# Optimization experiments

Hardware: AMD Instinct MI355X
Metric: run time of the kernel (lower is better)

The kernel has to match this reference:

```python
import jax, jax.numpy as jnp
import numpy as np
from jax import lax

B, NP = 4, 8192          # events, points per event (equal-sized batches)
RATIO, R, K = 0.25, 0.2, 64
MP = int(NP * RATIO)     # sampled centers per event
D_IN = 32
BIG = 1e10


def _fps_one(pos):
    # Farthest point sampling (deterministic start at index 0). pos: [NP,3] -> [MP] int32
    d = jnp.sum((pos - pos[0]) ** 2, axis=-1)
    sel = jnp.zeros((MP,), jnp.int32)

    def body(i, carry):
        sel, d = carry
        nxt = jnp.argmax(d).astype(jnp.int32)
        sel = sel.at[i].set(nxt)
        d = jnp.minimum(d, jnp.sum((pos - pos[nxt]) ** 2, axis=-1))
        return sel, d

    sel, _ = lax.fori_loop(1, MP, body, (sel, d))
    return sel


def _ball_query_one(centers, pos):
    # centers: [MP,3], pos: [NP,3] -> neighbor idx [MP,K] int32, validity mask [MP,K]
    d2 = jnp.sum((centers[:, None, :] - pos[None, :, :]) ** 2, axis=-1)  # [MP,NP]
    d2m = jnp.where(d2 <= R * R, d2, BIG)
    neg, idx = lax.top_k(-d2m, K)          # K nearest within radius (deterministic)
    mask = (-neg) <= R * R
    return idx.astype(jnp.int32), mask


def reference(x, pos, batch, W1, b1, W2, b2, W3, b3):
    xb = x.reshape(B, NP, D_IN)
    pb = pos.reshape(B, NP, 3)

    sel = jax.vmap(_fps_one)(pb)                                   # [B,MP]
    centers = jnp.take_along_axis(pb, sel[..., None], axis=1)      # [B,MP,3]
    idx, mask = jax.vmap(_ball_query_one)(centers, pb)             # [B,MP,K]

    gather = jax.vmap(lambda a, i: a[i])
    pos_j = gather(pb, idx)                                        # [B,MP,K,3]
    x_j = gather(xb, idx)                                          # [B,MP,K,D_IN]

    rel = pos_j - centers[:, :, None, :]
    h = jnp.concatenate([x_j, rel], axis=-1)                       # [B,MP,K,D_IN+3]
    h = jax.nn.relu(h @ W1 + b1)
    h = jax.nn.relu(h @ W2 + b2)
    h = jax.nn.relu(h @ W3 + b3)                                   # [B,MP,K,128]

    h = jnp.where(mask[..., None], h, -BIG)
    x_out = jnp.max(h, axis=2).reshape(B * MP, -1)                 # max aggregation
    pos_out = centers.reshape(B * MP, 3)
    batch_out = jnp.repeat(jnp.arange(B, dtype=jnp.int32), MP)
    return x_out, pos_out, batch_out


def setup_inputs() -> dict:
    key = jax.random.key(0)
    ks = jax.random.split(key, 8)
    x = jax.random.normal(ks[0], (B * NP, D_IN), jnp.float32)
    pos = jax.random.uniform(ks[1], (B * NP, 3), jnp.float32)
    batch = (jnp.arange(B * NP) // NP).astype(jnp.int64)
    W1 = jax.random.normal(ks[2], (D_IN + 3, 64), jnp.float32) * 0.05
    b1 = jnp.zeros((64,), jnp.float32)
    W2 = jax.random.normal(ks[3], (64, 64), jnp.float32) * 0.05
    b2 = jnp.zeros((64,), jnp.float32)
    W3 = jax.random.normal(ks[4], (64, 128), jnp.float32) * 0.05
    b3 = jnp.zeros((128,), jnp.float32)
    return {"x": x, "pos": pos, "batch": batch, "W1": W1, "b1": b1,
            "W2": W2, "b2": b2, "W3": W3, "b3": b3}
```

## Files before the change

### kernel.cpp

```cpp
#include <hip/hip_runtime.h>


#define BATCH 4
#define NP 8192
#define MP 2048
#define KNN 64
#define DIN 32

#define DPP_FMAX(v, ctrl)                                                     \
  {                                                                           \
    int _t = __builtin_amdgcn_update_dpp(__float_as_int(v),                   \
                                         __float_as_int(v), (ctrl), 0xF,      \
                                         0xF, false);                         \
    (v) = fmaxf((v), __int_as_float(_t));                                     \
  }

#define DPP_MINU(v, ctrl)                                                     \
  {                                                                           \
    unsigned _t = (unsigned)__builtin_amdgcn_update_dpp((int)(v), (int)(v),   \
                                                        (ctrl), 0xF, 0xF,    \
                                                        false);               \
    (v) = ((v) < _t) ? (v) : _t;                                              \
  }

#define DPP_WAVEMAX6(v)                                                       \
  {                                                                           \
    DPP_FMAX(v, 0x111);                                                       \
    DPP_FMAX(v, 0x112);                                                       \
    DPP_FMAX(v, 0x114);                                                       \
    DPP_FMAX(v, 0x118);                                                       \
    DPP_FMAX(v, 0x142);                                                       \
    DPP_FMAX(v, 0x143);                                                       \
  }

typedef float v2f __attribute__((ext_vector_type(2)));

__global__ __launch_bounds__(1024) void fps_k(const float* __restrict__ pos,
                                              const float* __restrict__ x,
                                              const float* __restrict__ W1,
                                              const float* __restrict__ W2,
                                              const float* __restrict__ W3,
                                              float* __restrict__ pout,
                                              float* __restrict__ bout,
                                              float* __restrict__ P1,
                                              float* __restrict__ W2T,
                                              float* __restrict__ W3T)
{
  const int bid = blockIdx.x;
  const int tid = threadIdx.x;

  if (bid >= BATCH) {
    if (bid < BATCH + 2048) {
      const int j = (bid - BATCH) * 16 + (tid >> 6);
      const int c = tid & 63;
      const float* __restrict__ xr = x + (size_t)j * DIN;
      float acc = 0.f;
#pragma unroll
      for (int k = 0; k < DIN; k++) acc += xr[k] * W1[k * 64 + c];
      P1[(size_t)j * 64 + c] = acc;
    } else {
#pragma unroll
      for (int it = 0; it < 12; it++) {
        const int e = it * 1024 + tid;
        if (e < 64 * 64) {
          const int c = e >> 6, k = e & 63;
          W2T[e] = W2[k * 64 + c];
        } else {
          const int e2 = e - 64 * 64;
          const int c = e2 >> 6, k = e2 & 63;
          W3T[e2] = W3[k * 128 + c];
        }
      }
    }
    return;
  }

  const int b = bid;
  const int lane = tid & 63, wid = tid >> 6;
  const float* __restrict__ pb = pos + (size_t)b * NP * 3;
  const int base = tid * 8;

  bout[b * MP + tid] = (float)b;
  bout[b * MP + 1024 + tid] = (float)b;

  __shared__ __align__(16) float ptab[NP * 3];
  __shared__ unsigned long long slt[2][16];

  float t[24];
  const float4* __restrict__ pv = (const float4*)(pb + (size_t)tid * 24);
#pragma unroll
  for (int q = 0; q < 6; q++) *(float4*)&t[q * 4] = pv[q];
#pragma unroll
  for (int q = 0; q < 6; q++) *(float4*)&ptab[tid * 24 + q * 4] = *(float4*)&t[q * 4];

  v2f px[4], py[4], pz[4], d[4];
#pragma unroll
  for (int j = 0; j < 4; j++) {
    px[j].x = t[6 * j + 0]; py[j].x = t[6 * j + 1]; pz[j].x = t[6 * j + 2];
    px[j].y = t[6 * j + 3]; py[j].y = t[6 * j + 4]; pz[j].y = t[6 * j + 5];
  }

  const float c0x = pb[0], c0y = pb[1], c0z = pb[2];
  if (tid == 0) {
    pout[(size_t)b * MP * 3 + 0] = c0x;
    pout[(size_t)b * MP * 3 + 1] = c0y;
    pout[(size_t)b * MP * 3 + 2] = c0z;
  }

  float bv = -1.f;
  {
    v2f cx = {c0x, c0x}, cy = {c0y, c0y}, cz = {c0z, c0z};
#pragma unroll
    for (int j = 0; j < 4; j++) {
      v2f dx = px[j] - cx, dy = py[j] - cy, dz = pz[j] - cz;
      v2f nd = dx * dx + dy * dy + dz * dz;
      d[j] = nd;
      bv = fmaxf(bv, fmaxf(nd.x, nd.y));
    }
  }

  for (int i = 1; i < MP; i++) {
    float v = bv;
    DPP_WAVEMAX6(v);
    const float wmax =
        __int_as_float(__builtin_amdgcn_readlane(__float_as_int(v), 63));

    const unsigned long long m = __ballot(bv == wmax);
    const int src = (int)__builtin_ctzll(m);
    const int p = i & 1;
    if (lane == src) {
      int ks = 7;
#pragma unroll
      for (int k = 6; k >= 0; k--) {
        float dv = (k & 1) ? d[k >> 1].y : d[k >> 1].x;
        if (dv == wmax) ks = k;
      }
      slt[p][wid] = ((unsigned long long)__float_as_uint(wmax) << 32)
                    | (unsigned)(base + ks);
    }
    __syncthreads();

    const unsigned long long kv = slt[p][lane & 15];
    const float v2 = __uint_as_float((unsigned)(kv >> 32));
    float v2r = v2;
    DPP_FMAX(v2r, 0x111);
    DPP_FMAX(v2r, 0x112);
    DPP_FMAX(v2r, 0x114);
    DPP_FMAX(v2r, 0x118);
    const float mv =
        __int_as_float(__builtin_amdgcn_readlane(__float_as_int(v2r), 15));
    const unsigned long long m2 = __ballot(v2 == mv);
    const int mw = (int)__builtin_ctzll(m2);
    const int js = __builtin_amdgcn_readlane((int)(unsigned)kv, mw);
    const float ncx = ptab[js * 3 + 0];
    const float ncy = ptab[js * 3 + 1];
    const float ncz = ptab[js * 3 + 2];

    if (tid == 0) {
      pout[((size_t)b * MP + i) * 3 + 0] = ncx;
      pout[((size_t)b * MP + i) * 3 + 1] = ncy;
      pout[((size_t)b * MP + i) * 3 + 2] = ncz;
    }

    const v2f cx = {ncx, ncx}, cy = {ncy, ncy}, cz = {ncz, ncz};
    bv = -1.f;
#pragma unroll
    for (int j = 0; j < 4; j++) {
      v2f dx = px[j] - cx, dy = py[j] - cy, dz = pz[j] - cz;
      v2f nd = dx * dx + dy * dy + dz * dz;
      v2f dn;
      dn.x = fminf(d[j].x, nd.x);
      dn.y = fminf(d[j].y, nd.y);
      d[j] = dn;
      bv = fmaxf(bv, fmaxf(dn.x, dn.y));
    }
  }
}

__global__ __launch_bounds__(64) void bqmlp_k(const float* __restrict__ pos,
    const float* __restrict__ P1, const float* __restrict__ W1,
    const float* __restrict__ b1, const float* __restrict__ W2T,
    const float* __restrict__ b2, const float* __restrict__ W3T,
    const float* __restrict__ b3, const float* __restrict__ pout,
    float* __restrict__ xout)
{
  __shared__ unsigned long long cand[1024];

  const int wg = blockIdx.x;
  const int lane = threadIdx.x;
  const int b = wg >> 11;
  const float* __restrict__ pb = pos + (size_t)b * NP * 3;
  const float cx = pout[(size_t)wg * 3 + 0];
  const float cy = pout[(size_t)wg * 3 + 1];
  const float cz = pout[(size_t)wg * 3 + 2];
  const float R2 = (float)(0.2 * 0.2);

  int cnt = 0;
  for (int basej = 0; basej < NP; basej += 64) {
    const int j = basej + lane;
    float dx = pb[j * 3 + 0] - cx;
    float dy = pb[j * 3 + 1] - cy;
    float dz = pb[j * 3 + 2] - cz;
    float d2 = dx * dx + dy * dy + dz * dz;
    bool in = (d2 <= R2);
    unsigned long long mb = __ballot(in);
    int pre = (int)__popcll(mb & ((1ull << lane) - 1ull));
    int slot = cnt + pre;
    if (in && slot < 1024)
      cand[slot] = ((unsigned long long)__float_as_uint(d2) << 32) | (unsigned int)j;
    cnt += (int)__popcll(mb);
  }
  if (cnt > 1024) cnt = 1024;

  unsigned long long last = 0;
  int myout = -1;
  for (int r = 0; r < KNN; r++) {
    unsigned long long v = ~0ull;
    for (int s = lane; s < cnt; s += 64) {
      const unsigned long long c = cand[s];
      if (c >= last && c < v) v = c;
    }
    const unsigned hi = (unsigned)(v >> 32);
    unsigned h = hi;
    DPP_MINU(h, 0x111);
    DPP_MINU(h, 0x112);
    DPP_MINU(h, 0x114);
    DPP_MINU(h, 0x118);
    DPP_MINU(h, 0x142);
    DPP_MINU(h, 0x143);
    const unsigned mhi = (unsigned)__builtin_amdgcn_readlane((int)h, 63);
    const unsigned lo = (hi == mhi) ? (unsigned)v : 0xffffffffu;
    unsigned l2 = lo;
    DPP_MINU(l2, 0x111);
    DPP_MINU(l2, 0x112);
    DPP_MINU(l2, 0x114);
    DPP_MINU(l2, 0x118);
    DPP_MINU(l2, 0x142);
    DPP_MINU(l2, 0x143);
    const unsigned mlo = (unsigned)__builtin_amdgcn_readlane((int)l2, 63);

    if (lane == r) myout = (mhi == 0xffffffffu) ? -1 : (int)mlo;
    last = (mhi == 0xffffffffu)
               ? ~0ull
               : ((((unsigned long long)mhi << 32) | mlo) + 1ull);
  }

  const int idx = myout;
  const bool valid = idx >= 0;
  const int j = valid ? idx : 0;
  const float* __restrict__ pj = pos + ((size_t)b * NP + j) * 3;
  const float rx = pj[0] - cx, ry = pj[1] - cy, rz = pj[2] - cz;
  const float* __restrict__ p1r =
      (const float*)__builtin_assume_aligned(P1 + ((size_t)b * NP + j) * 64, 16);

  float h1[64];
#pragma unroll
  for (int k = 0; k < 64; k++) {
    float v = p1r[k] + rx * W1[32 * 64 + k] + ry * W1[33 * 64 + k]
                     + rz * W1[34 * 64 + k] + b1[k];
    h1[k] = fmaxf(v, 0.f);
  }

  float h2[64];
#pragma unroll
  for (int c = 0; c < 64; c++) {
    float a = b2[c];
    const float* __restrict__ w = W2T + c * 64;
#pragma unroll
    for (int k = 0; k < 64; k++) a += h1[k] * w[k];
    h2[c] = fmaxf(a, 0.f);
  }

  float4 keep = make_float4(0.f, 0.f, 0.f, 0.f);
  for (int pass = 0; pass < 4; pass++) {
    const float* __restrict__ wp = W3T + (size_t)(pass * 32) * 64;
    const float* __restrict__ bp = b3 + pass * 32;
    float acc[32];
#pragma unroll
    for (int g = 0; g < 32; g++) acc[g] = bp[g];
#pragma unroll
    for (int k = 0; k < 64; k++) {
      const float hk = h2[k];
#pragma unroll
      for (int g = 0; g < 32; g++) acc[g] += hk * wp[g * 64 + k];
    }
#pragma unroll
    for (int g4 = 0; g4 < 8; g4++) {
      float a0 = valid ? fmaxf(acc[g4 * 4 + 0], 0.f) : 0.f;
      float a1 = valid ? fmaxf(acc[g4 * 4 + 1], 0.f) : 0.f;
      float a2 = valid ? fmaxf(acc[g4 * 4 + 2], 0.f) : 0.f;
      float a3 = valid ? fmaxf(acc[g4 * 4 + 3], 0.f) : 0.f;
      DPP_WAVEMAX6(a0);
      DPP_WAVEMAX6(a1);
      DPP_WAVEMAX6(a2);
      DPP_WAVEMAX6(a3);
      const float m0 =
          __int_as_float(__builtin_amdgcn_readlane(__float_as_int(a0), 63));
      const float m1 =
          __int_as_float(__builtin_amdgcn_readlane(__float_as_int(a1), 63));
      const float m2 =
          __int_as_float(__builtin_amdgcn_readlane(__float_as_int(a2), 63));
      const float m3 =
          __int_as_float(__builtin_amdgcn_readlane(__float_as_int(a3), 63));
      const int cch = pass * 8 + g4;
      if (lane == cch) {
        keep.x = m0; keep.y = m1; keep.z = m2; keep.w = m3;
      }
    }
  }
  if (lane < 32)
    *(float4*)&xout[(size_t)wg * 128 + lane * 4] = keep;
}

extern "C" void kernel_launch(void* const* d_in, const int* in_sizes, int n_in,
                              void* d_out, int out_size, void* d_ws, size_t ws_size,
                              hipStream_t stream)
{
  const float* x   = (const float*)d_in[0];
  const float* pos = (const float*)d_in[1];
  const float* W1 = (const float*)d_in[3];
  const float* b1 = (const float*)d_in[4];
  const float* W2 = (const float*)d_in[5];
  const float* b2 = (const float*)d_in[6];
  const float* W3 = (const float*)d_in[7];
  const float* b3 = (const float*)d_in[8];

  float* out  = (float*)d_out;
  float* xout = out;
  float* pout = out + 8192 * 128;
  float* bout = out + 8192 * 128 + 8192 * 3;

  char* ws = (char*)d_ws;
  float* P1  = (float*)ws;
  float* W2T = (float*)(ws + 8388608);
  float* W3T = (float*)(ws + 8404992);

  fps_k<<<dim3(BATCH + 2048 + 1), dim3(1024), 0, stream>>>(
      pos, x, W1, W2, W3, pout, bout, P1, W2T, W3T);
  bqmlp_k<<<dim3(BATCH * MP), dim3(64), 0, stream>>>(pos, P1, W1, b1, W2T, b2,
                                                     W3T, b3, pout, xout);
}
```

Before: 2.475 ms.

## Fuse FPS and ball-query MLP into persistent kernel overlapping via progress flags

```diff
diff --git a/kernel.cpp b/kernel.cpp
--- a/kernel.cpp
+++ b/kernel.cpp
@@ -6,6 +6,9 @@
 #define MP 2048
 #define KNN 64
 #define DIN 32
+#define NWORK 200
+#define NBLK (BATCH + NWORK)
+#define CAND_CAP 512
 
 #define DPP_FMAX(v, ctrl)                                                     \
   {                                                                           \
@@ -25,291 +28,311 @@
 
 #define DPP_WAVEMAX6(v)                                                       \
   {                                                                           \
-    DPP_FMAX(v, 0x111);                                                       \
-    DPP_FMAX(v, 0x112);                                                       \
-    DPP_FMAX(v, 0x114);                                                       \
-    DPP_FMAX(v, 0x118);                                                       \
-    DPP_FMAX(v, 0x142);                                                       \
-    DPP_FMAX(v, 0x143);                                                       \
+    DPP_FMAX(v, 0x111); DPP_FMAX(v, 0x112); DPP_FMAX(v, 0x114);               \
+    DPP_FMAX(v, 0x118); DPP_FMAX(v, 0x142); DPP_FMAX(v, 0x143);               \
+  }
+
+#define DPP_WAVEMINU6(v)                                                      \
+  {                                                                           \
+    DPP_MINU(v, 0x111); DPP_MINU(v, 0x112); DPP_MINU(v, 0x114);               \
+    DPP_MINU(v, 0x118); DPP_MINU(v, 0x142); DPP_MINU(v, 0x143);               \
   }
 
 typedef float v2f __attribute__((ext_vector_type(2)));
 
-__global__ __launch_bounds__(1024) void fps_k(const float* __restrict__ pos,
-                                              const float* __restrict__ x,
-                                              const float* __restrict__ W1,
-                                              const float* __restrict__ W2,
-                                              const float* __restrict__ W3,
-                                              float* __restrict__ pout,
-                                              float* __restrict__ bout,
-                                              float* __restrict__ P1,
-                                              float* __restrict__ W2T,
-                                              float* __restrict__ W3T)
+__device__ __forceinline__ int aload(const int* p) {
+  return __hip_atomic_load(p, __ATOMIC_RELAXED, __HIP_MEMORY_SCOPE_AGENT);
+}
+
+__global__ void init_k(int* __restrict__ flags) {
+  if (threadIdx.x < 8) flags[threadIdx.x] = 0;
+}
+
+__global__ __launch_bounds__(1024) void mega_k(const float* __restrict__ pos,
+                                               const float* __restrict__ x,
+                                               const float* __restrict__ W1,
+                                               const float* __restrict__ b1,
+                                               const float* __restrict__ W2,
+                                               const float* __restrict__ b2,
+                                               const float* __restrict__ W3,
+                                               const float* __restrict__ b3,
+                                               float* __restrict__ pout,
+                                               float* __restrict__ bout,
+                                               float* __restrict__ P1,
+                                               float* __restrict__ W2T,
+                                               float* __restrict__ xout,
+                                               int* __restrict__ flags)
 {
+  __shared__ __align__(16) float smem[NP * 3];
+  __shared__ unsigned long long slt[2][16];
+
+  int* const prog   = flags;
+  int* const ticket = flags + 4;
+  int* const p1done = flags + 5;
+
   const int bid = blockIdx.x;
   const int tid = threadIdx.x;
-
-  if (bid >= BATCH) {
-    if (bid < BATCH + 2048) {
-      const int j = (bid - BATCH) * 16 + (tid >> 6);
-      const int c = tid & 63;
+  const int lane = tid & 63, wid = tid >> 6;
+
+  if (bid < BATCH) {
+    const int b = bid;
+    float* const ptab = smem;
+    const float* __restrict__ pb = pos + (size_t)b * NP * 3;
+    const int base = tid * 8;
+
+    bout[b * MP + tid] = (float)b;
+    bout[b * MP + 1024 + tid] = (float)b;
+
+    float t[24];
+    const float4* __restrict__ pv = (const float4*)(pb + (size_t)tid * 24);
+#pragma unroll
+    for (int q = 0; q < 6; q++) *(float4*)&t[q * 4] = pv[q];
+#pragma unroll
+    for (int q = 0; q < 6; q++)
+      *(float4*)&ptab[tid * 24 + q * 4] = *(float4*)&t[q * 4];
+
+    v2f px[4], py[4], pz[4], d[4];
+#pragma unroll
+    for (int j = 0; j < 4; j++) {
+      px[j].x = t[6 * j + 0]; py[j].x = t[6 * j + 1]; pz[j].x = t[6 * j + 2];
+      px[j].y = t[6 * j + 3]; py[j].y = t[6 * j + 4]; pz[j].y = t[6 * j + 5];
+    }
+
+    const float c0x = pb[0], c0y = pb[1], c0z = pb[2];
+    if (tid == 0) {
+      pout[(size_t)b * MP * 3 + 0] = c0x;
+      pout[(size_t)b * MP * 3 + 1] = c0y;
+      pout[(size_t)b * MP * 3 + 2] = c0z;
+    }
+
+    float bv = -1.f;
+    {
+      v2f cx = {c0x, c0x}, cy = {c0y, c0y}, cz = {c0z, c0z};
+#pragma unroll
+      for (int j = 0; j < 4; j++) {
+        v2f dx = px[j] - cx, dy = py[j] - cy, dz = pz[j] - cz;
+        v2f nd = dx * dx + dy * dy + dz * dz;
+        d[j] = nd;
+        bv = fmaxf(bv, fmaxf(nd.x, nd.y));
+      }
+    }
+
+    for (int i = 1; i < MP; i++) {
+      float v = bv;
+      DPP_WAVEMAX6(v);
+      const float wmax =
+          __int_as_float(__builtin_amdgcn_readlane(__float_as_int(v), 63));
+
+      const unsigned long long m = __ballot(bv == wmax);
+      const int src = (int)__builtin_ctzll(m);
+      const int p = i & 1;
+      if (lane == src) {
+        int ks = 7;
+#pragma unroll
+        for (int k = 6; k >= 0; k--) {
+          float dv = (k & 1) ? d[k >> 1].y : d[k >> 1].x;
+          if (dv == wmax) ks = k;
+        }
+        slt[p][wid] = ((unsigned long long)__float_as_uint(wmax) << 32)
+                      | (unsigned)(base + ks);
+      }
+      __syncthreads();
+
+      const unsigned long long kv = slt[p][lane & 15];
+      const float v2 = __uint_as_float((unsigned)(kv >> 32));
+      float v2r = v2;
+      DPP_FMAX(v2r, 0x111);
+      DPP_FMAX(v2r, 0x112);
+      DPP_FMAX(v2r, 0x114);
+      DPP_FMAX(v2r, 0x118);
+      const float mv =
+          __int_as_float(__builtin_amdgcn_readlane(__float_as_int(v2r), 15));
+      const unsigned long long m2 = __ballot(v2 == mv);
+      const int mw = (int)__builtin_ctzll(m2);
+      const int js = __builtin_amdgcn_readlane((int)(unsigned)kv, mw);
+      const float ncx = ptab[js * 3 + 0];
+      const float ncy = ptab[js * 3 + 1];
+      const float ncz = ptab[js * 3 + 2];
+
+      if (tid == 0) {
+        pout[((size_t)b * MP + i) * 3 + 0] = ncx;
+        pout[((size_t)b * MP + i) * 3 + 1] = ncy;
+        pout[((size_t)b * MP + i) * 3 + 2] = ncz;
+        if ((i & 31) == 31) {
+          __threadfence();
+          __hip_atomic_store(&prog[b], i + 1, __ATOMIC_RELEASE,
+                             __HIP_MEMORY_SCOPE_AGENT);
+        }
+      }
+
+      const v2f cx = {ncx, ncx}, cy = {ncy, ncy}, cz = {ncz, ncz};
+      bv = -1.f;
+#pragma unroll
+      for (int j = 0; j < 4; j++) {
+        v2f dx = px[j] - cx, dy = py[j] - cy, dz = pz[j] - cz;
+        v2f nd = dx * dx + dy * dy + dz * dz;
+        v2f dn;
+        dn.x = fminf(d[j].x, nd.x);
+        dn.y = fminf(d[j].y, nd.y);
+        d[j] = dn;
+        bv = fmaxf(bv, fmaxf(dn.x, dn.y));
+      }
+    }
+    return;
+  }
+
+  {
+    const int wbid = bid - BATCH;
+    for (size_t e = (size_t)wbid * 1024 + tid; e < (size_t)32768 * 64;
+         e += (size_t)NWORK * 1024) {
+      const int j = (int)(e >> 6), c = (int)(e & 63);
       const float* __restrict__ xr = x + (size_t)j * DIN;
       float acc = 0.f;
 #pragma unroll
       for (int k = 0; k < DIN; k++) acc += xr[k] * W1[k * 64 + c];
       P1[(size_t)j * 64 + c] = acc;
-    } else {
-#pragma unroll
-      for (int it = 0; it < 12; it++) {
-        const int e = it * 1024 + tid;
-        if (e < 64 * 64) {
-          const int c = e >> 6, k = e & 63;
-          W2T[e] = W2[k * 64 + c];
-        } else {
-          const int e2 = e - 64 * 64;
-          const int c = e2 >> 6, k = e2 & 63;
-          W3T[e2] = W3[k * 128 + c];
+    }
+    if (bid == BATCH) {
+      for (int e = tid; e < 64 * 64; e += 1024) {
+        const int c = e >> 6, k = e & 63;
+        W2T[e] = W2[k * 64 + c];
+      }
+    }
+    __syncthreads();
+    if (tid == 0) { __threadfence(); atomicAdd(p1done, 1); }
+  }
+
+  unsigned long long* const cw =
+      (unsigned long long*)smem + (size_t)wid * CAND_CAP;
+  const float R2 = (float)(0.2 * 0.2);
+  bool mlp_ready = false;
+
+  for (;;) {
+    int t;
+    if (lane == 0) t = atomicAdd(ticket, 1);
+    t = __builtin_amdgcn_readfirstlane(t);
+    if (t >= BATCH * MP) break;
+    const int b = t & 3;
+    const int cIdx = t >> 2;
+    const int wg = b * MP + cIdx;
+
+    while (aload(&prog[b]) < cIdx + 1) __builtin_amdgcn_s_sleep(32);
+    __threadfence();
+
+    const float* __restrict__ pb = pos + (size_t)b * NP * 3;
+    const float cx = pout[(size_t)wg * 3 + 0];
+    const float cy = pout[(size_t)wg * 3 + 1];
+    const float cz = pout[(size_t)wg * 3 + 2];
+
+    int cnt = 0;
+    for (int basej = 0; basej < NP; basej += 64) {
+      const int j = basej + lane;
+      float dx = pb[j * 3 + 0] - cx;
+      float dy = pb[j * 3 + 1] - cy;
+      float dz = pb[j * 3 + 2] - cz;
+      float d2 = dx * dx + dy * dy + dz * dz;
+      bool in = (d2 <= R2);
+      unsigned long long mb = __ballot(in);
+      int pre = (int)__popcll(mb & ((1ull << lane) - 1ull));
+      int slot = cnt + pre;
+      if (in && slot < CAND_CAP)
+        cw[slot] = ((unsigned long long)__float_as_uint(d2) << 32)
+                   | (unsigned int)j;
+      cnt += (int)__popcll(mb);
+    }
+    if (cnt > CAND_CAP) cnt = CAND_CAP;
+
+    unsigned long long last = 0;
+    int myout = -1;
+    for (int r = 0; r < KNN; r++) {
+      unsigned long long v = ~0ull;
+      for (int s = lane; s < cnt; s += 64) {
+        const unsigned long long c = cw[s];
+        if (c >= last && c < v) v = c;
+      }
+      const unsigned hi = (unsigned)(v >> 32);
+      unsigned h = hi;
+      DPP_WAVEMINU6(h);
+      const unsigned mhi = (unsigned)__builtin_amdgcn_readlane((int)h, 63);
+      const unsigned lo = (hi == mhi) ? (unsigned)v : 0xffffffffu;
+      unsigned l2 = lo;
+      DPP_WAVEMINU6(l2);
+      const unsigned mlo = (unsigned)__builtin_amdgcn_readlane((int)l2, 63);
+      if (lane == r) myout = (mhi == 0xffffffffu) ? -1 : (int)mlo;
+      last = (mhi == 0xffffffffu)
+                 ? ~0ull
+                 : ((((unsigned long long)mhi << 32) | mlo) + 1ull);
+    }
+
+    if (!mlp_ready) {
+      while (aload(p1done) < NWORK) __builtin_amdgcn_s_sleep(32);
+      __threadfence();
+      mlp_ready = true;
+    }
+
+    const int idx = myout;
+    const bool valid = idx >= 0;
+    const int j = valid ? idx : 0;
+    const float* __restrict__ pj = pos + ((size_t)b * NP + j) * 3;
+    const float rx = pj[0] - cx, ry = pj[1] - cy, rz = pj[2] - cz;
+    const float* __restrict__ p1r = (const float*)__builtin_assume_aligned(
+        P1 + ((size_t)b * NP + j) * 64, 16);
+
+    float h1[64];
+#pragma unroll
+    for (int k = 0; k < 64; k++) {
+      float vv = p1r[k] + rx * W1[32 * 64 + k] + ry * W1[33 * 64 + k]
+                        + rz * W1[34 * 64 + k] + b1[k];
+      h1[k] = fmaxf(vv, 0.f);
+    }
+
+    float4 keep = make_float4(0.f, 0.f, 0.f, 0.f);
+    for (int pass = 0; pass < 4; pass++) {
+      float acc[32];
+#pragma unroll
+      for (int g = 0; g < 32; g++) acc[g] = b3[pass * 32 + g];
+#pragma unroll 2
+      for (int c = 0; c < 64; c++) {
+        const float* __restrict__ w = W2T + c * 64;
+        float a0 = 0.f, a1 = 0.f, a2 = 0.f, a3 = 0.f;
+#pragma unroll
+        for (int k4 = 0; k4 < 16; k4++) {
+          a0 += h1[k4 * 4 + 0] * w[k4 * 4 + 0];
+          a1 += h1[k4 * 4 + 1] * w[k4 * 4 + 1];
+          a2 += h1[k4 * 4 + 2] * w[k4 * 4 + 2];
+          a3 += h1[k4 * 4 + 3] * w[k4 * 4 + 3];
         }
-      }
-    }
-    return;
-  }
-
-  const int b = bid;
-  const int lane = tid & 63, wid = tid >> 6;
-  const float* __restrict__ pb = pos + (size_t)b * NP * 3;
-  const int base = tid * 8;
-
-  bout[b * MP + tid] = (float)b;
-  bout[b * MP + 1024 + tid] = (float)b;
-
-  __shared__ __align__(16) float ptab[NP * 3];
-  __shared__ unsigned long long slt[2][16];
-
-  float t[24];
-  const float4* __restrict__ pv = (const float4*)(pb + (size_t)tid * 24);
-#pragma unroll
-  for (int q = 0; q < 6; q++) *(float4*)&t[q * 4] = pv[q];
-#pragma unroll
-  for (int q = 0; q < 6; q++) *(float4*)&ptab[tid * 24 + q * 4] = *(float4*)&t[q * 4];
-
-  v2f px[4], py[4], pz[4], d[4];
-#pragma unroll
-  for (int j = 0; j < 4; j++) {
-    px[j].x = t[6 * j + 0]; py[j].x = t[6 * j + 1]; pz[j].x = t[6 * j + 2];
-    px[j].y = t[6 * j + 3]; py[j].y = t[6 * j + 4]; pz[j].y = t[6 * j + 5];
-  }
-
-  const float c0x = pb[0], c0y = pb[1], c0z = pb[2];
-  if (tid == 0) {
-    pout[(size_t)b * MP * 3 + 0] = c0x;
-    pout[(size_t)b * MP * 3 + 1] = c0y;
-    pout[(size_t)b * MP * 3 + 2] = c0z;
-  }
-
-  float bv = -1.f;
-  {
-    v2f cx = {c0x, c0x}, cy = {c0y, c0y}, cz = {c0z, c0z};
-#pragma unroll
-    for (int j = 0; j < 4; j++) {
-      v2f dx = px[j] - cx, dy = py[j] - cy, dz = pz[j] - cz;
-      v2f nd = dx * dx + dy * dy + dz * dz;
-      d[j] = nd;
-      bv = fmaxf(bv, fmaxf(nd.x, nd.y));
-    }
-  }
-
-  for (int i = 1; i < MP; i++) {
-    float v = bv;
-    DPP_WAVEMAX6(v);
-    const float wmax =
-        __int_as_float(__builtin_amdgcn_readlane(__float_as_int(v), 63));
-
-    const unsigned long long m = __ballot(bv == wmax);
-    const int src = (int)__builtin_ctzll(m);
-    const int p = i & 1;
-    if (lane == src) {
-      int ks = 7;
-#pragma unroll
-      for (int k = 6; k >= 0; k--) {
-        float dv = (k & 1) ? d[k >> 1].y : d[k >> 1].x;
-        if (dv == wmax) ks = k;
-      }
-      slt[p][wid] = ((unsigned long long)__float_as_uint(wmax) << 32)
-                    | (unsigned)(base + ks);
-    }
-    __syncthreads();
-
-    const unsigned long long kv = slt[p][lane & 15];
-    const float v2 = __uint_as_float((unsigned)(kv >> 32));
-    float v2r = v2;
-    DPP_FMAX(v2r, 0x111);
-    DPP_FMAX(v2r, 0x112);
-    DPP_FMAX(v2r, 0x114);
-    DPP_FMAX(v2r, 0x118);
-    const float mv =
-        __int_as_float(__builtin_amdgcn_readlane(__float_as_int(v2r), 15));
-    const unsigned long long m2 = __ballot(v2 == mv);
-    const int mw = (int)__builtin_ctzll(m2);
-    const int js = __builtin_amdgcn_readlane((int)(unsigned)kv, mw);
-    const float ncx = ptab[js * 3 + 0];
-    const float ncy = ptab[js * 3 + 1];
-    const float ncz = ptab[js * 3 + 2];
-
-    if (tid == 0) {
-      pout[((size_t)b * MP + i) * 3 + 0] = ncx;
-      pout[((size_t)b * MP + i) * 3 + 1] = ncy;
-      pout[((size_t)b * MP + i) * 3 + 2] = ncz;
-    }
-
-    const v2f cx = {ncx, ncx}, cy = {ncy, ncy}, cz = {ncz, ncz};
-    bv = -1.f;
-#pragma unroll
-    for (int j = 0; j < 4; j++) {
-      v2f dx = px[j] - cx, dy = py[j] - cy, dz = pz[j] - cz;
-      v2f nd = dx * dx + dy * dy + dz * dz;
-      v2f dn;
-      dn.x = fminf(d[j].x, nd.x);
-      dn.y = fminf(d[j].y, nd.y);
-      d[j] = dn;
-      bv = fmaxf(bv, fmaxf(dn.x, dn.y));
-    }
-  }
-}
-
-__global__ __launch_bounds__(64) void bqmlp_k(const float* __restrict__ pos,
-    const float* __restrict__ P1, const float* __restrict__ W1,
-    const float* __restrict__ b1, const float* __restrict__ W2T,
-    const float* __restrict__ b2, const float* __restrict__ W3T,
-    const float* __restrict__ b3, const float* __restrict__ pout,
-    float* __restrict__ xout)
-{
-  __shared__ unsigned long long cand[1024];
-
-  const int wg = blockIdx.x;
-  const int lane = threadIdx.x;
-  const int b = wg >> 11;
-  const float* __restrict__ pb = pos + (size_t)b * NP * 3;
-  const float cx = pout[(size_t)wg * 3 + 0];
-  const float cy = pout[(size_t)wg * 3 + 1];
-  const float cz = pout[(size_t)wg * 3 + 2];
-  const float R2 = (float)(0.2 * 0.2);
-
-  int cnt = 0;
-  for (int basej = 0; basej < NP; basej += 64) {
-    const int j = basej + lane;
-    float dx = pb[j * 3 + 0] - cx;
-    float dy = pb[j * 3 + 1] - cy;
-    float dz = pb[j * 3 + 2] - cz;
-    float d2 = dx * dx + dy * dy + dz * dz;
-    bool in = (d2 <= R2);
-    unsigned long long mb = __ballot(in);
-    int pre = (int)__popcll(mb & ((1ull << lane) - 1ull));
-    int slot = cnt + pre;
-    if (in && slot < 1024)
-      cand[slot] = ((unsigned long long)__float_as_uint(d2) << 32) | (unsigned int)j;
-    cnt += (int)__popcll(mb);
-  }
-  if (cnt > 1024) cnt = 1024;
-
-  unsigned long long last = 0;
-  int myout = -1;
-  for (int r = 0; r < KNN; r++) {
-    unsigned long long v = ~0ull;
-    for (int s = lane; s < cnt; s += 64) {
-      const unsigned long long c = cand[s];
-      if (c >= last && c < v) v = c;
-    }
-    const unsigned hi = (unsigned)(v >> 32);
-    unsigned h = hi;
-    DPP_MINU(h, 0x111);
-    DPP_MINU(h, 0x112);
-    DPP_MINU(h, 0x114);
-    DPP_MINU(h, 0x118);
-    DPP_MINU(h, 0x142);
-    DPP_MINU(h, 0x143);
-    const unsigned mhi = (unsigned)__builtin_amdgcn_readlane((int)h, 63);
-    const unsigned lo = (hi == mhi) ? (unsigned)v : 0xffffffffu;
-    unsigned l2 = lo;
-    DPP_MINU(l2, 0x111);
-    DPP_MINU(l2, 0x112);
-    DPP_MINU(l2, 0x114);
-    DPP_MINU(l2, 0x118);
-    DPP_MINU(l2, 0x142);
-    DPP_MINU(l2, 0x143);
-    const unsigned mlo = (unsigned)__builtin_amdgcn_readlane((int)l2, 63);
-
-    if (lane == r) myout = (mhi == 0xffffffffu) ? -1 : (int)mlo;
-    last = (mhi == 0xffffffffu)
-               ? ~0ull
-               : ((((unsigned long long)mhi << 32) | mlo) + 1ull);
-  }
-
-  const int idx = myout;
-  const bool valid = idx >= 0;
-  const int j = valid ? idx : 0;
-  const float* __restrict__ pj = pos + ((size_t)b * NP + j) * 3;
-  const float rx = pj[0] - cx, ry = pj[1] - cy, rz = pj[2] - cz;
-  const float* __restrict__ p1r =
-      (const float*)__builtin_assume_aligned(P1 + ((size_t)b * NP + j) * 64, 16);
-
-  float h1[64];
-#pragma unroll
-  for (int k = 0; k < 64; k++) {
-    float v = p1r[k] + rx * W1[32 * 64 + k] + ry * W1[33 * 64 + k]
-                     + rz * W1[34 * 64 + k] + b1[k];
-    h1[k] = fmaxf(v, 0.f);
-  }
-
-  float h2[64];
-#pragma unroll
-  for (int c = 0; c < 64; c++) {
-    float a = b2[c];
-    const float* __restrict__ w = W2T + c * 64;
-#pragma unroll
-    for (int k = 0; k < 64; k++) a += h1[k] * w[k];
-    h2[c] = fmaxf(a, 0.f);
-  }
-
-  float4 keep = make_float4(0.f, 0.f, 0.f, 0.f);
-  for (int pass = 0; pass < 4; pass++) {
-    const float* __restrict__ wp = W3T + (size_t)(pass * 32) * 64;
-    const float* __restrict__ bp = b3 + pass * 32;
-    float acc[32];
-#pragma unroll
-    for (int g = 0; g < 32; g++) acc[g] = bp[g];
-#pragma unroll
-    for (int k = 0; k < 64; k++) {
-      const float hk = h2[k];
-#pragma unroll
-      for (int g = 0; g < 32; g++) acc[g] += hk * wp[g * 64 + k];
-    }
-#pragma unroll
-    for (int g4 = 0; g4 < 8; g4++) {
-      float a0 = valid ? fmaxf(acc[g4 * 4 + 0], 0.f) : 0.f;
-      float a1 = valid ? fmaxf(acc[g4 * 4 + 1], 0.f) : 0.f;
-      float a2 = valid ? fmaxf(acc[g4 * 4 + 2], 0.f) : 0.f;
-      float a3 = valid ? fmaxf(acc[g4 * 4 + 3], 0.f) : 0.f;
-      DPP_WAVEMAX6(a0);
-      DPP_WAVEMAX6(a1);
-      DPP_WAVEMAX6(a2);
-      DPP_WAVEMAX6(a3);
-      const float m0 =
-          __int_as_float(__builtin_amdgcn_readlane(__float_as_int(a0), 63));
-      const float m1 =
-          __int_as_float(__builtin_amdgcn_readlane(__float_as_int(a1), 63));
-      const float m2 =
-          __int_as_float(__builtin_amdgcn_readlane(__float_as_int(a2), 63));
-      const float m3 =
-          __int_as_float(__builtin_amdgcn_readlane(__float_as_int(a3), 63));
-      const int cch = pass * 8 + g4;
-      if (lane == cch) {
-        keep.x = m0; keep.y = m1; keep.z = m2; keep.w = m3;
-      }
-    }
-  }
-  if (lane < 32)
-    *(float4*)&xout[(size_t)wg * 128 + lane * 4] = keep;
+        const float h2c = fmaxf(b2[c] + ((a0 + a1) + (a2 + a3)), 0.f);
+        const float* __restrict__ w3r = W3 + c * 128 + pass * 32;
+#pragma unroll
+        for (int g = 0; g < 32; g++) acc[g] += h2c * w3r[g];
+      }
+#pragma unroll
+      for (int g4 = 0; g4 < 8; g4++) {
+        float a0 = valid ? fmaxf(acc[g4 * 4 + 0], 0.f) : 0.f;
+        float a1 = valid ? fmaxf(acc[g4 * 4 + 1], 0.f) : 0.f;
+        float a2 = valid ? fmaxf(acc[g4 * 4 + 2], 0.f) : 0.f;
+        float a3 = valid ? fmaxf(acc[g4 * 4 + 3], 0.f) : 0.f;
+        DPP_WAVEMAX6(a0);
+        DPP_WAVEMAX6(a1);
+        DPP_WAVEMAX6(a2);
+        DPP_WAVEMAX6(a3);
+        const float m0 =
+            __int_as_float(__builtin_amdgcn_readlane(__float_as_int(a0), 63));
+        const float m1 =
+            __int_as_float(__builtin_amdgcn_readlane(__float_as_int(a1), 63));
+        const float m2 =
+            __int_as_float(__builtin_amdgcn_readlane(__float_as_int(a2), 63));
+        const float m3 =
+            __int_as_float(__builtin_amdgcn_readlane(__float_as_int(a3), 63));
+        if (lane == pass * 8 + g4) {
+          keep.x = m0; keep.y = m1; keep.z = m2; keep.w = m3;
+        }
+      }
+    }
+    if (lane < 32)
+      *(float4*)&xout[(size_t)wg * 128 + lane * 4] = keep;
+  }
 }
 
 extern "C" void kernel_launch(void* const* d_in, const int* in_sizes, int n_in,
@@ -331,12 +354,12 @@
   float* bout = out + 8192 * 128 + 8192 * 3;
 
   char* ws = (char*)d_ws;
-  float* P1  = (float*)ws;
-  float* W2T = (float*)(ws + 8388608);
-  float* W3T = (float*)(ws + 8404992);
-
-  fps_k<<<dim3(BATCH + 2048 + 1), dim3(1024), 0, stream>>>(
-      pos, x, W1, W2, W3, pout, bout, P1, W2T, W3T);
-  bqmlp_k<<<dim3(BATCH * MP), dim3(64), 0, stream>>>(pos, P1, W1, b1, W2T, b2,
-                                                     W3T, b3, pout, xout);
+  float* P1    = (float*)ws;
+  float* W2T   = (float*)(ws + 8388608);
+  int*   flags = (int*)(ws + 8404992);
+
+  init_k<<<dim3(1), dim3(64), 0, stream>>>(flags);
+  mega_k<<<dim3(NBLK), dim3(1024), 0, stream>>>(pos, x, W1, b1, W2, b2, W3,
+                                                b3, pout, bout, P1, W2T,
+                                                xout, flags);
 }
```

Result: faster. 2.426 ms (-2.0%).
